# Performance work log

Hardware: AMD Instinct MI355X
Metric: run time of the kernel (lower is better)

The kernel has to match this reference:

```python
import jax, jax.numpy as jnp
import numpy as np

B, T, D, H = 4, 1024, 1024, 16
HD = D // H
DFF = 2048          # ExpertTier hidden width
K = 3               # ConvTier causal kernel size
NEG = -1e9


def layernorm(x, w, b, eps=1e-5):
    m = jnp.mean(x, axis=-1, keepdims=True)
    v = jnp.var(x, axis=-1, keepdims=True)
    return (x - m) * jax.lax.rsqrt(v + eps) * w + b


def rope_cos_sin(t, hd):
    inv = 1.0 / (10000.0 ** (jnp.arange(0, hd, 2, dtype=jnp.float32) / hd))
    freqs = jnp.outer(jnp.arange(t, dtype=jnp.float32), inv)  # (T, hd/2)
    return jnp.cos(freqs), jnp.sin(freqs)


def apply_rope(x, cos, sin):
    # x: (B, H, T, hd); cos/sin: (T, hd/2)
    x1, x2 = jnp.split(x, 2, axis=-1)
    return jnp.concatenate([x1 * cos - x2 * sin, x1 * sin + x2 * cos], axis=-1)


def causal_attn(q, k, v):
    # q,k,v: (..., T, d); full causal softmax attention
    t = q.shape[-2]
    scale = 1.0 / jnp.sqrt(jnp.asarray(q.shape[-1], q.dtype))
    scores = jnp.einsum('...qd,...kd->...qk', q, k) * scale
    mask = jnp.triu(jnp.ones((t, t), dtype=bool), k=1)
    scores = jnp.where(mask, NEG, scores)
    w = jax.nn.softmax(scores, axis=-1)
    return jnp.einsum('...qk,...kd->...qd', w, v)


def setup_inputs() -> dict:
    key = jax.random.key(0)
    ks = jax.random.split(key, 16)
    ws = 0.02
    g = lambda k, shape, s: jax.random.normal(k, shape, dtype=jnp.float32) * s
    return {
        'x': g(ks[0], (B, T, D), 1.0),
        'ln1_w': jnp.ones((D,), jnp.float32), 'ln1_b': jnp.zeros((D,), jnp.float32),
        'qkv_w': g(ks[1], (D, 3 * D), ws),
        'out_w': g(ks[2], (D, D), ws),
        'ln2_w': jnp.ones((D,), jnp.float32), 'ln2_b': jnp.zeros((D,), jnp.float32),
        'router_w': g(ks[3], (D, 4), ws),
        'conv_w': g(ks[4], (D, 1, K), 0.1),             # depthwise OIW, groups=D
        'expert_w1': g(ks[5], (D, DFF), ws),
        'expert_w2': g(ks[6], (DFF, D), ws),
        'at_wq': g(ks[7], (D, D), ws),
        'at_wk': g(ks[8], (D, D), ws),
        'at_wv': g(ks[9], (D, D), ws),
        'at_wo': g(ks[10], (D, D), ws),
        'tier_gate': jnp.full((D,), 0.1, jnp.float32),
        'sink_kv_scale': jnp.asarray(0.1, jnp.float32),
    }


def reference(x, ln1_w, ln1_b, qkv_w, out_w, ln2_w, ln2_b, router_w, conv_w,
              expert_w1, expert_w2, at_wq, at_wk, at_wv, at_wo,
              tier_gate, sink_kv_scale):
    b, t, d = x.shape
    # --- backbone causal self-attention with RoPE (pre-norm) ---
    h1 = layernorm(x, ln1_w, ln1_b)
    qkv = (h1 @ qkv_w).reshape(b, t, 3, H, HD)
    q = qkv[:, :, 0].transpose(0, 2, 1, 3)  # (B,H,T,hd)
    k = qkv[:, :, 1].transpose(0, 2, 1, 3)
    v = qkv[:, :, 2].transpose(0, 2, 1, 3)
    cos, sin = rope_cos_sin(t, HD)
    q = apply_rope(q, cos, sin)
    k = apply_rope(k, cos, sin)
    ao = causal_attn(q, k, v)                         # (B,H,T,hd)
    ao = ao.transpose(0, 2, 1, 3).reshape(b, t, d) @ out_w
    x = x + ao
    # --- router + tiers ---
    h = layernorm(x, ln2_w, ln2_b)
    routing_w = jax.nn.softmax(h @ router_w, axis=-1)  # (B,T,4): conv/expert/attn/sink
    # ConvTier: depthwise causal conv (k=3) + GELU
    hc = jnp.pad(h.transpose(0, 2, 1), ((0, 0), (0, 0), (K - 1, 0)))  # (B,D,T+K-1)
    conv = jax.lax.conv_general_dilated(hc, conv_w, (1,), 'VALID',
                                        feature_group_count=d,
                                        dimension_numbers=('NCH', 'OIH', 'NCH'))
    conv_out = jax.nn.gelu(conv.transpose(0, 2, 1))   # (B,T,D)
    # ExpertTier: 2-layer GELU MLP
    expert_out = jax.nn.gelu(h @ expert_w1) @ expert_w2
    # AttentionTier: single-head causal attention
    attn2 = causal_attn(h @ at_wq, h @ at_wk, h @ at_wv) @ at_wo
    # SinkTier outputs zeros -> contributes nothing to the weighted sum
    combined = (conv_out * routing_w[..., 0:1]
                + expert_out * routing_w[..., 1:2]
                + attn2 * routing_w[..., 2:3])
    x = x + combined * tier_gate
    # sink kv scaling
    kv_scale = 1.0 - routing_w[..., 3] * (1.0 - jnp.abs(sink_kv_scale))
    x = x * kv_scale[..., None]
    return (x, routing_w)
```

## Files before the change

kernel.cpp:

```cpp
#include <hip/hip_runtime.h>

#define Bz 4
#define Tz 1024
#define Dz 1024
#define Hz 16
#define NTz (Bz*Tz)

typedef short s8v __attribute__((ext_vector_type(8)));
typedef float f4v __attribute__((ext_vector_type(4)));

__device__ __forceinline__ float bf2f(unsigned short u){
  unsigned int x = ((unsigned int)u) << 16;
  return __builtin_bit_cast(float, x);
}
__device__ __forceinline__ unsigned short f2bf(float f){
  unsigned int x = __builtin_bit_cast(unsigned int, f);
  x += 0x7fffu + ((x >> 16) & 1u);
  return (unsigned short)(x >> 16);
}
__device__ __forceinline__ float gelu_f(float x){
  float z = 1.5957691216057308f * (x + 0.044715f * x * x * x);
  return x / (1.0f + __expf(-z));
}
__device__ __forceinline__ void gl16(const unsigned short* g, unsigned short* l){
  __builtin_amdgcn_global_load_lds(
      (const __attribute__((address_space(1))) unsigned int*)g,
      (__attribute__((address_space(3))) unsigned int*)l, 16, 0, 0);
}

__global__ __launch_bounds__(256) void k_convtrans(const float* __restrict__ in,
    unsigned short* __restrict__ out, int R, int C)
{
  __shared__ float tile[32][33];
  int c0 = blockIdx.x * 32, r0 = blockIdx.y * 32;
  int tx = threadIdx.x & 31, ty = threadIdx.x >> 5;
  #pragma unroll
  for (int i = 0; i < 32; i += 8)
    tile[ty + i][tx] = in[(long)(r0 + ty + i) * C + c0 + tx];
  __syncthreads();
  #pragma unroll
  for (int i = 0; i < 32; i += 8)
    out[(long)(c0 + ty + i) * R + r0 + tx] = f2bf(tile[tx][ty + i]);
}

__global__ __launch_bounds__(256) void k_convtrans_b(const unsigned short* __restrict__ in,
    unsigned short* __restrict__ out, int ld, long sIn, long sOut)
{
  __shared__ unsigned short tile[32][34];
  in  += (long)blockIdx.z * sIn;
  out += (long)blockIdx.z * sOut;
  int c0 = blockIdx.x * 32, r0 = blockIdx.y * 32;
  int tx = threadIdx.x & 31, ty = threadIdx.x >> 5;
  #pragma unroll
  for (int i = 0; i < 32; i += 8)
    tile[ty + i][tx] = in[(long)(r0 + ty + i) * ld + c0 + tx];
  __syncthreads();
  #pragma unroll
  for (int i = 0; i < 32; i += 8)
    out[(long)(c0 + ty + i) * 1024 + r0 + tx] = tile[tx][ty + i];
}

__global__ __launch_bounds__(256) void k_layernorm(const float* __restrict__ x,
    const float* __restrict__ w, const float* __restrict__ b,
    unsigned short* __restrict__ out)
{
  int row = blockIdx.x, tid = threadIdx.x;
  const float4* xp = (const float4*)(x + (long)row * Dz);
  float4 v = xp[tid];
  float s  = v.x + v.y + v.z + v.w;
  float ss = v.x*v.x + v.y*v.y + v.z*v.z + v.w*v.w;
  int lane = tid & 63, wv = tid >> 6;
  #pragma unroll
  for (int off = 32; off; off >>= 1){ s += __shfl_xor(s, off); ss += __shfl_xor(ss, off); }
  __shared__ float red[8];
  if (lane == 0){ red[wv] = s; red[4 + wv] = ss; }
  __syncthreads();
  s  = red[0] + red[1] + red[2] + red[3];
  ss = red[4] + red[5] + red[6] + red[7];
  float mean = s * (1.0f / Dz);
  float var  = ss * (1.0f / Dz) - mean * mean;
  float rstd = rsqrtf(var + 1e-5f);
  float4 wg = ((const float4*)w)[tid];
  float4 bg = ((const float4*)b)[tid];
  ushort4 ov;
  ov.x = f2bf((v.x - mean) * rstd * wg.x + bg.x);
  ov.y = f2bf((v.y - mean) * rstd * wg.y + bg.y);
  ov.z = f2bf((v.z - mean) * rstd * wg.z + bg.z);
  ov.w = f2bf((v.w - mean) * rstd * wg.w + bg.w);
  *((ushort4*)(out + (long)row * Dz) + tid) = ov;
}

template<int MODE, int BN, bool TRIMAP, bool TRIK, bool DBUF>
__global__ __launch_bounds__(256) void k_gemm(
    const unsigned short* __restrict__ A,
    const unsigned short* __restrict__ Bt,
    float* __restrict__ Cf, unsigned short* __restrict__ Cb,
    const float* __restrict__ addsrc,
    unsigned short* __restrict__ P1, unsigned short* __restrict__ P2,
    int N, int K, int lda, int ldb,
    long sA, long sB, long sC)
{
  constexpr int BM = 128;
  constexpr int MREP = (BN == 128) ? 4 : 2;
  constexpr int NB = DBUF ? 2 : 1;
  __shared__ unsigned short As[NB][BM * 64];
  __shared__ unsigned short Bs[NB][BN * 64];
  int bm, bn;
  if (TRIMAP) {
    int li = blockIdx.x;
    int nwg = gridDim.x;
    if ((nwg & 7) == 0) li = (li & 7) * (nwg >> 3) + (li >> 3);
    int r = (int)((sqrtf(4.f * li + 1.f) - 1.f) * 0.5f);
    if ((r + 1) * (r + 2) <= li) ++r;
    if (r * (r + 1) > li) --r;
    bm = r * 128; bn = (li - r * (r + 1)) * BN;
  } else {
    int lin = blockIdx.y * gridDim.x + blockIdx.x;
    int nwg = gridDim.x * gridDim.y;
    if ((nwg & 7) == 0) lin = (lin & 7) * (nwg >> 3) + (lin >> 3);
    bm = (lin / gridDim.x) * BM; bn = (lin % gridDim.x) * BN;
  }
  A  += (long)blockIdx.z * sA;
  Bt += (long)blockIdx.z * sB;
  int tid = threadIdx.x, w = tid >> 6, lane = tid & 63;
  int wr, wc;
  if (BN == 128) { wr = (w >> 1) * 64; wc = (w & 1) * 64; }
  else           { wr = w * 32;        wc = 0; }
  f4v acc[MREP][4];
  #pragma unroll
  for (int m = 0; m < MREP; ++m)
    #pragma unroll
    for (int n = 0; n < 4; ++n)
      acc[m][n] = (f4v){0.f, 0.f, 0.f, 0.f};

  int Keff = K;
  if (TRIK) Keff = min(K, bm + BM);

  int lrow = lane >> 3;
  int lcol = (((lane & 7) ^ lrow) * 8);
  const unsigned short* AgJ[4];
  int AsOff[4];
  #pragma unroll
  for (int j = 0; j < 4; ++j) {
    AgJ[j] = A + (long)(bm + w * 32 + j * 8 + lrow) * lda + lcol;
    AsOff[j] = (w * 32 + j * 8) * 64;
  }
  constexpr int BCH = BN / 8 / 4;
  const unsigned short* BgJ[BCH];
  int BsOff[BCH];
  #pragma unroll
  for (int j = 0; j < BCH; ++j) {
    BgJ[j] = Bt + (long)(bn + w * (BCH * 8) + j * 8 + lrow) * ldb + lcol;
    BsOff[j] = (w * (BCH * 8) + j * 8) * 64;
  }

  int fr = lane & 15, fg = lane >> 4;
  int sw = (fr & 7) * 8;

  auto stage = [&](int buf, int k0){
    #pragma unroll
    for (int j = 0; j < 4; ++j) gl16(AgJ[j] + k0, &As[buf][AsOff[j]]);
    #pragma unroll
    for (int j = 0; j < BCH; ++j) gl16(BgJ[j] + k0, &Bs[buf][BsOff[j]]);
  };
  auto compute = [&](int buf){
    #pragma unroll
    for (int kk = 0; kk < 2; ++kk) {
      int kg = (kk * 32 + fg * 8) ^ sw;
      s8v af[MREP], bfv[4];
      #pragma unroll
      for (int m = 0; m < MREP; ++m) af[m]  = *(const s8v*)&As[buf][(wr + m * 16 + fr) * 64 + kg];
      #pragma unroll
      for (int n = 0; n < 4; ++n)    bfv[n] = *(const s8v*)&Bs[buf][(wc + n * 16 + fr) * 64 + kg];
      #pragma unroll
      for (int m = 0; m < MREP; ++m)
        #pragma unroll
        for (int n = 0; n < 4; ++n)
          acc[m][n] = __builtin_amdgcn_mfma_f32_16x16x32_bf16(af[m], bfv[n], acc[m][n], 0, 0, 0);
    }
  };

  if (DBUF) {
    int cur = 0;
    stage(0, 0);
    __syncthreads();
    for (int k0 = 0; k0 < Keff; k0 += 64) {
      if (k0 + 64 < Keff) stage(cur ^ 1, k0 + 64);
      compute(cur);
      __syncthreads();
      cur ^= 1;
    }
  } else {
    for (int k0 = 0; k0 < Keff; k0 += 64) {
      __syncthreads();
      stage(0, k0);
      __syncthreads();
      compute(0);
    }
  }

  int cr0 = bm + wr + fg * 4;
  int cc0 = bn + wc + fr;

  if (MODE == 4) {
    int sect = bn >> 10;
    if (sect == 2) {
      #pragma unroll
      for (int m = 0; m < MREP; ++m)
        #pragma unroll
        for (int n = 0; n < 4; ++n)
          #pragma unroll
          for (int i = 0; i < 4; ++i) {
            int row = cr0 + m * 16 + i;
            int vcol = (bn - 2048) + wc + n * 16 + fr;
            P2[(long)row * 1024 + vcol] = f2bf(acc[m][n][i]);
          }
    } else {
      unsigned short* dst = (sect == 0) ? Cb : P1;
      float scl = (sect == 0) ? 0.125f : 1.0f;
      int head = ((bn & 1023) + wc) >> 6;
      float inv0 = exp2f(-(float)fr * 0.4152410118609203f);
      float inv1 = exp2f(-(float)(fr + 16) * 0.4152410118609203f);
      #pragma unroll
      for (int m = 0; m < MREP; ++m)
        #pragma unroll
        for (int i = 0; i < 4; ++i) {
          int row = cr0 + m * 16 + i;
          int t = row & 1023, bq = row >> 10;
          float a0 = (float)t * inv0, a1 = (float)t * inv1;
          float cs0 = __cosf(a0), sn0 = __sinf(a0);
          float cs1 = __cosf(a1), sn1 = __sinf(a1);
          float v0 = acc[m][0][i], v1 = acc[m][1][i];
          float v2 = acc[m][2][i], v3 = acc[m][3][i];
          long base = ((long)(bq * 16 + head)) * 65536 + (long)t * 64 + fr;
          dst[base]      = f2bf((v0 * cs0 - v2 * sn0) * scl);
          dst[base + 32] = f2bf((v0 * sn0 + v2 * cs0) * scl);
          dst[base + 16] = f2bf((v1 * cs1 - v3 * sn1) * scl);
          dst[base + 48] = f2bf((v1 * sn1 + v3 * cs1) * scl);
        }
    }
    return;
  }

  #pragma unroll
  for (int m = 0; m < MREP; ++m)
    #pragma unroll
    for (int n = 0; n < 4; ++n)
      #pragma unroll
      for (int i = 0; i < 4; ++i) {
        long row = cr0 + m * 16 + i, col = cc0 + n * 16;
        long idx = (long)blockIdx.z * sC + row * (long)N + col;
        float v = acc[m][n][i];
        if (MODE == 1) v += addsrc[idx];
        if (MODE == 5) { if (col < 2048) v = gelu_f(v); }
        if (MODE <= 1) Cf[idx] = v; else Cb[idx] = f2bf(v);
      }
}

__global__ __launch_bounds__(256) void k_attn_mfma(
    const unsigned short* __restrict__ Qb, const unsigned short* __restrict__ Kb,
    const unsigned short* __restrict__ Vt, unsigned short* __restrict__ ao)
{
  __shared__ unsigned short Ks[64][72];
  __shared__ unsigned short Vs[64][72];
  __shared__ unsigned short Ps[4][16][72];
  int qb = 15 - (blockIdx.x >> 6);
  int bh = blockIdx.x & 63;
  int b = bh >> 4, h = bh & 15;
  int t0 = qb * 64;
  int tid = threadIdx.x, w = tid >> 6, lane = tid & 63;
  int fr = lane & 15, fg = lane >> 4;

  const unsigned short* qp = Qb + (long)bh * Tz * 64 + (long)(t0 + w * 16 + fr) * 64 + fg * 8;
  s8v qf[2] = { *(const s8v*)qp, *(const s8v*)(qp + 32) };

  f4v o_acc[4];
  #pragma unroll
  for (int n = 0; n < 4; ++n) o_acc[n] = (f4v){0.f, 0.f, 0.f, 0.f};
  float m_[4] = {-1e30f, -1e30f, -1e30f, -1e30f};
  float l_[4] = {0.f, 0.f, 0.f, 0.f};

  int sr = tid >> 3, sc = (tid & 7) * 8;
  const unsigned short* Kg = Kb + (long)bh * Tz * 64 + (long)sr * 64 + sc;
  const unsigned short* Vg = Vt + (long)bh * 64 * Tz + (long)sr * Tz + sc;

  for (int kt = 0; kt <= qb; ++kt) {
    int k0 = kt * 64;
    __syncthreads();
    *(uint4*)&Ks[sr][sc]      = *(const uint4*)(Kg + (long)k0 * 64);
    *(uint4*)&Ks[sr + 32][sc] = *(const uint4*)(Kg + (long)(k0 + 32) * 64);
    *(uint4*)&Vs[sr][sc]      = *(const uint4*)(Vg + k0);
    *(uint4*)&Vs[sr + 32][sc] = *(const uint4*)(Vg + (long)32 * Tz + k0);
    __syncthreads();

    f4v sacc[4];
    #pragma unroll
    for (int n = 0; n < 4; ++n) sacc[n] = (f4v){0.f, 0.f, 0.f, 0.f};
    #pragma unroll
    for (int kk = 0; kk < 2; ++kk) {
      int kg = kk * 32 + fg * 8;
      #pragma unroll
      for (int n = 0; n < 4; ++n) {
        s8v bf = *(const s8v*)&Ks[n * 16 + fr][kg];
        sacc[n] = __builtin_amdgcn_mfma_f32_16x16x32_bf16(qf[kk], bf, sacc[n], 0, 0, 0);
      }
    }

    bool full = (kt < qb);
    float p[4][4], alpha[4];
    #pragma unroll
    for (int i = 0; i < 4; ++i) {
      int trow = t0 + w * 16 + fg * 4 + i;
      float mx = -1e30f;
      #pragma unroll
      for (int n = 0; n < 4; ++n) {
        float sval = sacc[n][i];
        if (!full) {
          int key = k0 + n * 16 + fr;
          sval = (key <= trow) ? sval : -1e30f;
        }
        p[n][i] = sval;
        mx = fmaxf(mx, sval);
      }
      mx = fmaxf(mx, __shfl_xor(mx, 1));
      mx = fmaxf(mx, __shfl_xor(mx, 2));
      mx = fmaxf(mx, __shfl_xor(mx, 4));
      mx = fmaxf(mx, __shfl_xor(mx, 8));
      float mnew = fmaxf(m_[i], mx);
      alpha[i] = __expf(m_[i] - mnew);
      m_[i] = mnew;
      float ps = 0.f;
      #pragma unroll
      for (int n = 0; n < 4; ++n) {
        float pv = __expf(p[n][i] - mnew);
        p[n][i] = pv;
        ps += pv;
      }
      ps += __shfl_xor(ps, 1); ps += __shfl_xor(ps, 2);
      ps += __shfl_xor(ps, 4); ps += __shfl_xor(ps, 8);
      l_[i] = l_[i] * alpha[i] + ps;
    }
    #pragma unroll
    for (int n = 0; n < 4; ++n)
      #pragma unroll
      for (int i = 0; i < 4; ++i)
        o_acc[n][i] *= alpha[i];
    #pragma unroll
    for (int n = 0; n < 4; ++n)
      #pragma unroll
      for (int i = 0; i < 4; ++i)
        Ps[w][fg * 4 + i][n * 16 + fr] = f2bf(p[n][i]);

    #pragma unroll
    for (int kk = 0; kk < 2; ++kk) {
      int kg = kk * 32 + fg * 8;
      s8v pa = *(const s8v*)&Ps[w][fr][kg];
      #pragma unroll
      for (int n = 0; n < 4; ++n) {
        s8v vb = *(const s8v*)&Vs[n * 16 + fr][kg];
        o_acc[n] = __builtin_amdgcn_mfma_f32_16x16x32_bf16(pa, vb, o_acc[n], 0, 0, 0);
      }
    }
  }

  float inv[4];
  #pragma unroll
  for (int i = 0; i < 4; ++i) inv[i] = 1.0f / l_[i];
  #pragma unroll
  for (int n = 0; n < 4; ++n)
    #pragma unroll
    for (int i = 0; i < 4; ++i) {
      int t = t0 + w * 16 + fg * 4 + i;
      ao[((long)(b * Tz + t)) * Dz + h * 64 + n * 16 + fr] = f2bf(o_acc[n][i] * inv[i]);
    }
}

__global__ __launch_bounds__(256) void k_router(const unsigned short* __restrict__ h,
    const float* __restrict__ rw, float* __restrict__ rout)
{
  int row = blockIdx.x, tid = threadIdx.x;
  float a0 = 0.f, a1 = 0.f, a2 = 0.f, a3 = 0.f;
  const unsigned short* hp = h + (long)row * Dz;
  for (int d = tid; d < Dz; d += 256) {
    float hv = bf2f(hp[d]);
    float4 w4 = *(const float4*)(rw + d * 4);
    a0 = fmaf(hv, w4.x, a0); a1 = fmaf(hv, w4.y, a1);
    a2 = fmaf(hv, w4.z, a2); a3 = fmaf(hv, w4.w, a3);
  }
  int lane = tid & 63, wv = tid >> 6;
  #pragma unroll
  for (int off = 32; off; off >>= 1) {
    a0 += __shfl_xor(a0, off); a1 += __shfl_xor(a1, off);
    a2 += __shfl_xor(a2, off); a3 += __shfl_xor(a3, off);
  }
  __shared__ float red[4][4];
  if (lane == 0){ red[wv][0] = a0; red[wv][1] = a1; red[wv][2] = a2; red[wv][3] = a3; }
  __syncthreads();
  if (tid == 0) {
    float s0 = red[0][0] + red[1][0] + red[2][0] + red[3][0];
    float s1 = red[0][1] + red[1][1] + red[2][1] + red[3][1];
    float s2 = red[0][2] + red[1][2] + red[2][2] + red[3][2];
    float s3 = red[0][3] + red[1][3] + red[2][3] + red[3][3];
    float mx = fmaxf(fmaxf(s0, s1), fmaxf(s2, s3));
    float e0 = __expf(s0 - mx), e1 = __expf(s1 - mx);
    float e2 = __expf(s2 - mx), e3 = __expf(s3 - mx);
    float inv = 1.0f / (e0 + e1 + e2 + e3);
    float4 r = {e0 * inv, e1 * inv, e2 * inv, e3 * inv};
    *(float4*)(rout + (long)row * 4) = r;
  }
}

__global__ __launch_bounds__(256) void k_softmax_causal(const float* __restrict__ S,
    unsigned short* __restrict__ P, float scale)
{
  long row = blockIdx.x;
  int t = (int)(row & (Tz - 1));
  int tid = threadIdx.x;
  const float* sp = S + row * Tz;
  float4 v = *(const float4*)(sp + tid * 4);
  float vv[4];
  vv[0] = (tid*4 + 0 <= t) ? v.x * scale : -1e30f;
  vv[1] = (tid*4 + 1 <= t) ? v.y * scale : -1e30f;
  vv[2] = (tid*4 + 2 <= t) ? v.z * scale : -1e30f;
  vv[3] = (tid*4 + 3 <= t) ? v.w * scale : -1e30f;
  float mx = fmaxf(fmaxf(vv[0], vv[1]), fmaxf(vv[2], vv[3]));
  int lane = tid & 63, wv = tid >> 6;
  #pragma unroll
  for (int off = 32; off; off >>= 1) mx = fmaxf(mx, __shfl_xor(mx, off));
  __shared__ float red[8];
  if (lane == 0) red[wv] = mx;
  __syncthreads();
  mx = fmaxf(fmaxf(red[0], red[1]), fmaxf(red[2], red[3]));
  float p[4];
  float s = 0.f;
  #pragma unroll
  for (int i = 0; i < 4; ++i){ p[i] = __expf(vv[i] - mx); s += p[i]; }
  #pragma unroll
  for (int off = 32; off; off >>= 1) s += __shfl_xor(s, off);
  if (lane == 0) red[4 + wv] = s;
  __syncthreads();
  s = red[4] + red[5] + red[6] + red[7];
  float inv = 1.0f / s;
  ushort4 ov;
  ov.x = f2bf(p[0] * inv); ov.y = f2bf(p[1] * inv);
  ov.z = f2bf(p[2] * inv); ov.w = f2bf(p[3] * inv);
  *((ushort4*)(P + row * Tz) + tid) = ov;
}

__global__ __launch_bounds__(256) void k_combine(
    const float* __restrict__ x2, const unsigned short* __restrict__ hbf,
    const float* __restrict__ eo, const float* __restrict__ ap,
    const float* __restrict__ rout, const float* __restrict__ convw,
    const float* __restrict__ tg, const float* __restrict__ sinkp,
    float* __restrict__ outx)
{
  int row = blockIdx.x, tid = threadIdx.x;
  int t = row & (Tz - 1), b = row >> 10;
  int d0 = tid * 4;
  float4 x4 = *(const float4*)(x2 + (long)row * Dz + d0);
  float4 e4 = *(const float4*)(eo + (long)row * Dz + d0);
  float4 a4 = *(const float4*)(ap + (long)row * Dz + d0);
  float4 t4 = *(const float4*)(tg + d0);
  float4 r4 = *(const float4*)(rout + (long)row * 4);
  float sks = fabsf(sinkp[0]);
  float kv = 1.0f - r4.w * (1.0f - sks);
  const float4* cwp = (const float4*)(convw + (long)d0 * 3);
  float4 c0 = cwp[0], c1 = cwp[1], c2 = cwp[2];
  float cwf[12] = {c0.x, c0.y, c0.z, c0.w, c1.x, c1.y, c1.z, c1.w, c2.x, c2.y, c2.z, c2.w};
  float hv[3][4];
  #pragma unroll
  for (int tap = 0; tap < 3; ++tap) {
    int tt = t - 2 + tap;
    if (tt >= 0) {
      ushort4 hu = *((const ushort4*)(hbf + ((long)(b * Tz + tt)) * Dz + d0));
      hv[tap][0] = bf2f(hu.x); hv[tap][1] = bf2f(hu.y);
      hv[tap][2] = bf2f(hu.z); hv[tap][3] = bf2f(hu.w);
    } else {
      hv[tap][0] = 0.f; hv[tap][1] = 0.f; hv[tap][2] = 0.f; hv[tap][3] = 0.f;
    }
  }
  float ov[4];
  float xi[4] = {x4.x, x4.y, x4.z, x4.w};
  float ei[4] = {e4.x, e4.y, e4.z, e4.w};
  float ai[4] = {a4.x, a4.y, a4.z, a4.w};
  float ti[4] = {t4.x, t4.y, t4.z, t4.w};
  #pragma unroll
  for (int i = 0; i < 4; ++i) {
    float conv = hv[0][i] * cwf[i*3 + 0] + hv[1][i] * cwf[i*3 + 1] + hv[2][i] * cwf[i*3 + 2];
    float comb = gelu_f(conv) * r4.x + ei[i] * r4.y + ai[i] * r4.z;
    ov[i] = (xi[i] + comb * ti[i]) * kv;
  }
  float4 res = {ov[0], ov[1], ov[2], ov[3]};
  *(float4*)(outx + (long)row * Dz + d0) = res;
}

extern "C" void kernel_launch(void* const* d_in, const int* in_sizes, int n_in,
                              void* d_out, int out_size, void* d_ws, size_t ws_size,
                              hipStream_t stream) {
  (void)in_sizes; (void)n_in; (void)out_size; (void)ws_size;
  const float* x       = (const float*)d_in[0];
  const float* ln1_w   = (const float*)d_in[1];
  const float* ln1_b   = (const float*)d_in[2];
  const float* qkv_w   = (const float*)d_in[3];
  const float* out_w   = (const float*)d_in[4];
  const float* ln2_w   = (const float*)d_in[5];
  const float* ln2_b   = (const float*)d_in[6];
  const float* router_w= (const float*)d_in[7];
  const float* conv_w  = (const float*)d_in[8];
  const float* ew1     = (const float*)d_in[9];
  const float* ew2     = (const float*)d_in[10];
  const float* at_wq   = (const float*)d_in[11];
  const float* at_wk   = (const float*)d_in[12];
  const float* at_wv   = (const float*)d_in[13];
  const float* at_wo   = (const float*)d_in[14];
  const float* tg      = (const float*)d_in[15];
  const float* sinkp   = (const float*)d_in[16];
  float* outx = (float*)d_out;
  float* rout = outx + (size_t)NTz * Dz;

  char* ws = (char*)d_ws;
  size_t off = 0;
  auto alloc = [&](size_t bytes) -> char* {
    char* p = ws + off;
    off += (bytes + 255) & ~(size_t)255;
    return p;
  };
  const long TD = (long)Tz * Dz, TT = (long)Tz * Tz;

  unsigned short* w_qkvt  = (unsigned short*)alloc((size_t)3072*1024*2);
  unsigned short* w_outt  = (unsigned short*)alloc((size_t)1024*1024*2);
  unsigned short* w_tiert = (unsigned short*)alloc((size_t)5120*1024*2);
  unsigned short* w_ew2t  = (unsigned short*)alloc((size_t)1024*2048*2);
  unsigned short* w_wot   = (unsigned short*)alloc((size_t)1024*1024*2);
  unsigned short* h1bf    = (unsigned short*)alloc((size_t)NTz*Dz*2);
  unsigned short* tierb   = (unsigned short*)alloc((size_t)NTz*5120*2);
  unsigned short* aobf    = (unsigned short*)alloc((size_t)NTz*Dz*2);
  float*          x2f     = (float*)alloc((size_t)NTz*Dz*4);
  unsigned short* hbf     = (unsigned short*)alloc((size_t)NTz*Dz*2);
  unsigned short* Pbf     = (unsigned short*)alloc((size_t)Bz*Tz*Tz*2);
  unsigned short* v2tbf   = (unsigned short*)alloc((size_t)NTz*Dz*2);
  unsigned short* a2obf   = (unsigned short*)alloc((size_t)NTz*Dz*2);
  float*          eof_    = (float*)alloc((size_t)NTz*Dz*4);
  float*          a2pf    = (float*)alloc((size_t)NTz*Dz*4);
  float*          Sf      = (float*)alloc((size_t)Bz*Tz*Tz*4);

  unsigned short* Qb = (unsigned short*)x2f;
  unsigned short* Kb = Pbf;
  unsigned short* Vb = tierb;
  unsigned short* Vt = (unsigned short*)a2pf;

  dim3 blk(256);

  k_convtrans<<<dim3(96, 32), blk, 0, stream>>>(qkv_w, w_qkvt, 1024, 3072);
  k_convtrans<<<dim3(32, 32), blk, 0, stream>>>(out_w, w_outt, 1024, 1024);
  k_convtrans<<<dim3(64, 32), blk, 0, stream>>>(ew1,   w_tiert,                 1024, 2048);
  k_convtrans<<<dim3(32, 32), blk, 0, stream>>>(at_wq, w_tiert + 2048*1024,     1024, 1024);
  k_convtrans<<<dim3(32, 32), blk, 0, stream>>>(at_wk, w_tiert + 3072*1024,     1024, 1024);
  k_convtrans<<<dim3(32, 32), blk, 0, stream>>>(at_wv, w_tiert + (size_t)4096*1024, 1024, 1024);
  k_convtrans<<<dim3(32, 64), blk, 0, stream>>>(ew2,   w_ew2t, 2048, 1024);
  k_convtrans<<<dim3(32, 32), blk, 0, stream>>>(at_wo, w_wot, 1024, 1024);

  k_layernorm<<<NTz, blk, 0, stream>>>(x, ln1_w, ln1_b, h1bf);
  k_gemm<4,128,false,false,false><<<dim3(24, 32), blk, 0, stream>>>(h1bf, w_qkvt,
      nullptr, Qb, nullptr, Kb, Vb, 3072, 1024, 1024, 1024, 0, 0, 0);
  k_convtrans_b<<<dim3(32, 32, 4), blk, 0, stream>>>(Vb, Vt, 1024, TD, TD);
  k_attn_mfma<<<dim3(1024), blk, 0, stream>>>(Qb, Kb, Vt, aobf);
  k_gemm<1,64,false,false,true><<<dim3(16, 32), blk, 0, stream>>>(aobf, w_outt, x2f,
      nullptr, x, nullptr, nullptr, 1024, 1024, 1024, 1024, 0, 0, 0);
  k_layernorm<<<NTz, blk, 0, stream>>>(x2f, ln2_w, ln2_b, hbf);
  k_router<<<NTz, blk, 0, stream>>>(hbf, router_w, rout);
  k_gemm<5,128,false,false,false><<<dim3(40, 32), blk, 0, stream>>>(hbf, w_tiert,
      nullptr, tierb, nullptr, nullptr, nullptr, 5120, 1024, 1024, 1024, 0, 0, 0);
  k_gemm<0,64,false,false,true><<<dim3(16, 32), blk, 0, stream>>>(tierb, w_ew2t, eof_,
      nullptr, nullptr, nullptr, nullptr, 1024, 2048, 5120, 2048, 0, 0, 0);
  k_convtrans_b<<<dim3(32, 32, 4), blk, 0, stream>>>(tierb + 4096, v2tbf, 5120,
      (long)Tz*5120, TD);
  k_gemm<0,64,true,false,true><<<dim3(72, 1, 4), blk, 0, stream>>>(tierb + 2048,
      tierb + 3072, Sf, nullptr, nullptr, nullptr, nullptr,
      1024, 1024, 5120, 5120, (long)Tz*5120, (long)Tz*5120, TT);
  k_softmax_causal<<<NTz, blk, 0, stream>>>(Sf, Pbf, 0.03125f);
  k_gemm<3,64,false,true,true><<<dim3(16, 8, 4), blk, 0, stream>>>(Pbf, v2tbf, nullptr,
      a2obf, nullptr, nullptr, nullptr, 1024, 1024, 1024, 1024, TT, TD, TD);
  k_gemm<0,64,false,false,true><<<dim3(16, 32), blk, 0, stream>>>(a2obf, w_wot, a2pf,
      nullptr, nullptr, nullptr, nullptr, 1024, 1024, 1024, 1024, 0, 0, 0);
  k_combine<<<NTz, blk, 0, stream>>>(x2f, hbf, eof_, a2pf, rout, conv_w, tg, sinkp, outx);
}
```

Baseline: 313.5 us.

## Fuse LN2 with router, store intermediates in bf16, add grouped tile swizzle

Merges the second layernorm and the router projection into one kernel, which removes a launch and a re-read of the normalized activations. The expert output, attention projection and score matrix are now stored as bf16 instead of fp32, with the score scaling folded into the GEMM epilogue, cutting write and read traffic. The GEMM block mapping switches to grouped-M tile ordering, reversing the row order for the triangular-K case, to improve L2 reuse and load balance. Storing scores and intermediates in bf16 lowers precision before the softmax and the final combine.

```diff
diff --git a/kernel.cpp b/kernel.cpp
--- a/kernel.cpp
+++ b/kernel.cpp
@@ -88,6 +88,67 @@
   ov.z = f2bf((v.z - mean) * rstd * wg.z + bg.z);
   ov.w = f2bf((v.w - mean) * rstd * wg.w + bg.w);
   *((ushort4*)(out + (long)row * Dz) + tid) = ov;
+}
+
+__global__ __launch_bounds__(256) void k_ln_router(const float* __restrict__ x,
+    const float* __restrict__ w, const float* __restrict__ b,
+    const float* __restrict__ rw, unsigned short* __restrict__ out,
+    float* __restrict__ rout)
+{
+  int row = blockIdx.x, tid = threadIdx.x;
+  const float4* xp = (const float4*)(x + (long)row * Dz);
+  float4 v = xp[tid];
+  float s  = v.x + v.y + v.z + v.w;
+  float ss = v.x*v.x + v.y*v.y + v.z*v.z + v.w*v.w;
+  int lane = tid & 63, wv = tid >> 6;
+  #pragma unroll
+  for (int off = 32; off; off >>= 1){ s += __shfl_xor(s, off); ss += __shfl_xor(ss, off); }
+  __shared__ float red[8];
+  if (lane == 0){ red[wv] = s; red[4 + wv] = ss; }
+  __syncthreads();
+  s  = red[0] + red[1] + red[2] + red[3];
+  ss = red[4] + red[5] + red[6] + red[7];
+  float mean = s * (1.0f / Dz);
+  float var  = ss * (1.0f / Dz) - mean * mean;
+  float rstd = rsqrtf(var + 1e-5f);
+  float4 wg = ((const float4*)w)[tid];
+  float4 bg = ((const float4*)b)[tid];
+  float h0 = (v.x - mean) * rstd * wg.x + bg.x;
+  float h1 = (v.y - mean) * rstd * wg.y + bg.y;
+  float h2 = (v.z - mean) * rstd * wg.z + bg.z;
+  float h3 = (v.w - mean) * rstd * wg.w + bg.w;
+  ushort4 ov;
+  ov.x = f2bf(h0); ov.y = f2bf(h1); ov.z = f2bf(h2); ov.w = f2bf(h3);
+  *((ushort4*)(out + (long)row * Dz) + tid) = ov;
+  int d0 = tid * 4;
+  float4 r0 = *(const float4*)(rw + (long)d0 * 4);
+  float4 r1 = *(const float4*)(rw + (long)(d0 + 1) * 4);
+  float4 r2 = *(const float4*)(rw + (long)(d0 + 2) * 4);
+  float4 r3 = *(const float4*)(rw + (long)(d0 + 3) * 4);
+  float a0 = h0*r0.x + h1*r1.x + h2*r2.x + h3*r3.x;
+  float a1 = h0*r0.y + h1*r1.y + h2*r2.y + h3*r3.y;
+  float a2 = h0*r0.z + h1*r1.z + h2*r2.z + h3*r3.z;
+  float a3 = h0*r0.w + h1*r1.w + h2*r2.w + h3*r3.w;
+  #pragma unroll
+  for (int off = 32; off; off >>= 1) {
+    a0 += __shfl_xor(a0, off); a1 += __shfl_xor(a1, off);
+    a2 += __shfl_xor(a2, off); a3 += __shfl_xor(a3, off);
+  }
+  __shared__ float red2[4][4];
+  if (lane == 0){ red2[wv][0] = a0; red2[wv][1] = a1; red2[wv][2] = a2; red2[wv][3] = a3; }
+  __syncthreads();
+  if (tid == 0) {
+    float s0 = red2[0][0] + red2[1][0] + red2[2][0] + red2[3][0];
+    float s1 = red2[0][1] + red2[1][1] + red2[2][1] + red2[3][1];
+    float s2 = red2[0][2] + red2[1][2] + red2[2][2] + red2[3][2];
+    float s3 = red2[0][3] + red2[1][3] + red2[2][3] + red2[3][3];
+    float mx = fmaxf(fmaxf(s0, s1), fmaxf(s2, s3));
+    float e0 = __expf(s0 - mx), e1 = __expf(s1 - mx);
+    float e2 = __expf(s2 - mx), e3 = __expf(s3 - mx);
+    float inv = 1.0f / (e0 + e1 + e2 + e3);
+    float4 r = {e0 * inv, e1 * inv, e2 * inv, e3 * inv};
+    *(float4*)(rout + (long)row * 4) = r;
+  }
 }
 
 template<int MODE, int BN, bool TRIMAP, bool TRIK, bool DBUF>
@@ -118,7 +179,17 @@
     int lin = blockIdx.y * gridDim.x + blockIdx.x;
     int nwg = gridDim.x * gridDim.y;
     if ((nwg & 7) == 0) lin = (lin & 7) * (nwg >> 3) + (lin >> 3);
-    bm = (lin / gridDim.x) * BM; bn = (lin % gridDim.x) * BN;
+    int cols = gridDim.x, rows = gridDim.y;
+    constexpr int GM = 8;
+    int in_grp = GM * cols;
+    int gid = lin / in_grp;
+    int fm = gid * GM;
+    int gsz = min(rows - fm, GM);
+    int rem = lin - gid * in_grp;
+    int pm = fm + (rem % gsz);
+    int pn = rem / gsz;
+    if (TRIK) pm = rows - 1 - pm;
+    bm = pm * BM; bn = pn * BN;
   }
   A  += (long)blockIdx.z * sA;
   Bt += (long)blockIdx.z * sB;
@@ -253,6 +324,7 @@
         float v = acc[m][n][i];
         if (MODE == 1) v += addsrc[idx];
         if (MODE == 5) { if (col < 2048) v = gelu_f(v); }
+        if (MODE == 6) v *= 0.03125f;
         if (MODE <= 1) Cf[idx] = v; else Cb[idx] = f2bf(v);
       }
 }
@@ -375,54 +447,19 @@
     }
 }
 
-__global__ __launch_bounds__(256) void k_router(const unsigned short* __restrict__ h,
-    const float* __restrict__ rw, float* __restrict__ rout)
-{
-  int row = blockIdx.x, tid = threadIdx.x;
-  float a0 = 0.f, a1 = 0.f, a2 = 0.f, a3 = 0.f;
-  const unsigned short* hp = h + (long)row * Dz;
-  for (int d = tid; d < Dz; d += 256) {
-    float hv = bf2f(hp[d]);
-    float4 w4 = *(const float4*)(rw + d * 4);
-    a0 = fmaf(hv, w4.x, a0); a1 = fmaf(hv, w4.y, a1);
-    a2 = fmaf(hv, w4.z, a2); a3 = fmaf(hv, w4.w, a3);
-  }
-  int lane = tid & 63, wv = tid >> 6;
-  #pragma unroll
-  for (int off = 32; off; off >>= 1) {
-    a0 += __shfl_xor(a0, off); a1 += __shfl_xor(a1, off);
-    a2 += __shfl_xor(a2, off); a3 += __shfl_xor(a3, off);
-  }
-  __shared__ float red[4][4];
-  if (lane == 0){ red[wv][0] = a0; red[wv][1] = a1; red[wv][2] = a2; red[wv][3] = a3; }
-  __syncthreads();
-  if (tid == 0) {
-    float s0 = red[0][0] + red[1][0] + red[2][0] + red[3][0];
-    float s1 = red[0][1] + red[1][1] + red[2][1] + red[3][1];
-    float s2 = red[0][2] + red[1][2] + red[2][2] + red[3][2];
-    float s3 = red[0][3] + red[1][3] + red[2][3] + red[3][3];
-    float mx = fmaxf(fmaxf(s0, s1), fmaxf(s2, s3));
-    float e0 = __expf(s0 - mx), e1 = __expf(s1 - mx);
-    float e2 = __expf(s2 - mx), e3 = __expf(s3 - mx);
-    float inv = 1.0f / (e0 + e1 + e2 + e3);
-    float4 r = {e0 * inv, e1 * inv, e2 * inv, e3 * inv};
-    *(float4*)(rout + (long)row * 4) = r;
-  }
-}
-
-__global__ __launch_bounds__(256) void k_softmax_causal(const float* __restrict__ S,
-    unsigned short* __restrict__ P, float scale)
+__global__ __launch_bounds__(256) void k_softmax_causal(const unsigned short* __restrict__ S,
+    unsigned short* __restrict__ P)
 {
   long row = blockIdx.x;
   int t = (int)(row & (Tz - 1));
   int tid = threadIdx.x;
-  const float* sp = S + row * Tz;
-  float4 v = *(const float4*)(sp + tid * 4);
+  const unsigned short* sp = S + row * Tz;
+  ushort4 v = ((const ushort4*)sp)[tid];
   float vv[4];
-  vv[0] = (tid*4 + 0 <= t) ? v.x * scale : -1e30f;
-  vv[1] = (tid*4 + 1 <= t) ? v.y * scale : -1e30f;
-  vv[2] = (tid*4 + 2 <= t) ? v.z * scale : -1e30f;
-  vv[3] = (tid*4 + 3 <= t) ? v.w * scale : -1e30f;
+  vv[0] = (tid*4 + 0 <= t) ? bf2f(v.x) : -1e30f;
+  vv[1] = (tid*4 + 1 <= t) ? bf2f(v.y) : -1e30f;
+  vv[2] = (tid*4 + 2 <= t) ? bf2f(v.z) : -1e30f;
+  vv[3] = (tid*4 + 3 <= t) ? bf2f(v.w) : -1e30f;
   float mx = fmaxf(fmaxf(vv[0], vv[1]), fmaxf(vv[2], vv[3]));
   int lane = tid & 63, wv = tid >> 6;
   #pragma unroll
@@ -449,7 +486,7 @@
 
 __global__ __launch_bounds__(256) void k_combine(
     const float* __restrict__ x2, const unsigned short* __restrict__ hbf,
-    const float* __restrict__ eo, const float* __restrict__ ap,
+    const unsigned short* __restrict__ eo, const unsigned short* __restrict__ ap,
     const float* __restrict__ rout, const float* __restrict__ convw,
     const float* __restrict__ tg, const float* __restrict__ sinkp,
     float* __restrict__ outx)
@@ -458,8 +495,8 @@
   int t = row & (Tz - 1), b = row >> 10;
   int d0 = tid * 4;
   float4 x4 = *(const float4*)(x2 + (long)row * Dz + d0);
-  float4 e4 = *(const float4*)(eo + (long)row * Dz + d0);
-  float4 a4 = *(const float4*)(ap + (long)row * Dz + d0);
+  ushort4 e4 = *(const ushort4*)(eo + (long)row * Dz + d0);
+  ushort4 a4 = *(const ushort4*)(ap + (long)row * Dz + d0);
   float4 t4 = *(const float4*)(tg + d0);
   float4 r4 = *(const float4*)(rout + (long)row * 4);
   float sks = fabsf(sinkp[0]);
@@ -481,8 +518,8 @@
   }
   float ov[4];
   float xi[4] = {x4.x, x4.y, x4.z, x4.w};
-  float ei[4] = {e4.x, e4.y, e4.z, e4.w};
-  float ai[4] = {a4.x, a4.y, a4.z, a4.w};
+  float ei[4] = {bf2f(e4.x), bf2f(e4.y), bf2f(e4.z), bf2f(e4.w)};
+  float ai[4] = {bf2f(a4.x), bf2f(a4.y), bf2f(a4.z), bf2f(a4.w)};
   float ti[4] = {t4.x, t4.y, t4.z, t4.w};
   #pragma unroll
   for (int i = 0; i < 4; ++i) {
@@ -540,14 +577,14 @@
   unsigned short* Pbf     = (unsigned short*)alloc((size_t)Bz*Tz*Tz*2);
   unsigned short* v2tbf   = (unsigned short*)alloc((size_t)NTz*Dz*2);
   unsigned short* a2obf   = (unsigned short*)alloc((size_t)NTz*Dz*2);
-  float*          eof_    = (float*)alloc((size_t)NTz*Dz*4);
-  float*          a2pf    = (float*)alloc((size_t)NTz*Dz*4);
-  float*          Sf      = (float*)alloc((size_t)Bz*Tz*Tz*4);
+  unsigned short* eofb    = (unsigned short*)alloc((size_t)NTz*Dz*2);
+  unsigned short* a2pb    = (unsigned short*)alloc((size_t)NTz*Dz*2);
+  unsigned short* Sbf     = (unsigned short*)alloc((size_t)Bz*Tz*Tz*2);
 
   unsigned short* Qb = (unsigned short*)x2f;
   unsigned short* Kb = Pbf;
   unsigned short* Vb = tierb;
-  unsigned short* Vt = (unsigned short*)a2pf;
+  unsigned short* Vt = a2pb;
 
   dim3 blk(256);
 
@@ -567,21 +604,20 @@
   k_attn_mfma<<<dim3(1024), blk, 0, stream>>>(Qb, Kb, Vt, aobf);
   k_gemm<1,64,false,false,true><<<dim3(16, 32), blk, 0, stream>>>(aobf, w_outt, x2f,
       nullptr, x, nullptr, nullptr, 1024, 1024, 1024, 1024, 0, 0, 0);
-  k_layernorm<<<NTz, blk, 0, stream>>>(x2f, ln2_w, ln2_b, hbf);
-  k_router<<<NTz, blk, 0, stream>>>(hbf, router_w, rout);
+  k_ln_router<<<NTz, blk, 0, stream>>>(x2f, ln2_w, ln2_b, router_w, hbf, rout);
   k_gemm<5,128,false,false,false><<<dim3(40, 32), blk, 0, stream>>>(hbf, w_tiert,
       nullptr, tierb, nullptr, nullptr, nullptr, 5120, 1024, 1024, 1024, 0, 0, 0);
-  k_gemm<0,64,false,false,true><<<dim3(16, 32), blk, 0, stream>>>(tierb, w_ew2t, eof_,
-      nullptr, nullptr, nullptr, nullptr, 1024, 2048, 5120, 2048, 0, 0, 0);
+  k_gemm<3,64,false,false,true><<<dim3(16, 32), blk, 0, stream>>>(tierb, w_ew2t, nullptr,
+      eofb, nullptr, nullptr, nullptr, 1024, 2048, 5120, 2048, 0, 0, 0);
   k_convtrans_b<<<dim3(32, 32, 4), blk, 0, stream>>>(tierb + 4096, v2tbf, 5120,
       (long)Tz*5120, TD);
-  k_gemm<0,64,true,false,true><<<dim3(72, 1, 4), blk, 0, stream>>>(tierb + 2048,
-      tierb + 3072, Sf, nullptr, nullptr, nullptr, nullptr,
+  k_gemm<6,64,true,false,true><<<dim3(72, 1, 4), blk, 0, stream>>>(tierb + 2048,
+      tierb + 3072, nullptr, Sbf, nullptr, nullptr, nullptr,
       1024, 1024, 5120, 5120, (long)Tz*5120, (long)Tz*5120, TT);
-  k_softmax_causal<<<NTz, blk, 0, stream>>>(Sf, Pbf, 0.03125f);
+  k_softmax_causal<<<NTz, blk, 0, stream>>>(Sbf, Pbf);
   k_gemm<3,64,false,true,true><<<dim3(16, 8, 4), blk, 0, stream>>>(Pbf, v2tbf, nullptr,
       a2obf, nullptr, nullptr, nullptr, 1024, 1024, 1024, 1024, TT, TD, TD);
-  k_gemm<0,64,false,false,true><<<dim3(16, 32), blk, 0, stream>>>(a2obf, w_wot, a2pf,
-      nullptr, nullptr, nullptr, nullptr, 1024, 1024, 1024, 1024, 0, 0, 0);
-  k_combine<<<NTz, blk, 0, stream>>>(x2f, hbf, eof_, a2pf, rout, conv_w, tg, sinkp, outx);
-}
+  k_gemm<3,64,false,false,true><<<dim3(16, 32), blk, 0, stream>>>(a2obf, w_wot, nullptr,
+      a2pb, nullptr, nullptr, nullptr, 1024, 1024, 1024, 1024, 0, 0, 0);
+  k_combine<<<NTz, blk, 0, stream>>>(x2f, hbf, eofb, a2pb, rout, conv_w, tg, sinkp, outx);
+}
```

Measured after the change: 306.2 us. 1.02x faster.
